# Performance work log

Hardware: AMD Instinct MI355X
Metric: run time of the kernel (lower is better)

The kernel has to match this reference:

```python
import jax, jax.numpy as jnp
import numpy as np

D_MODEL = 1024
NHEAD = 16
D_K = D_MODEL // NHEAD


def setup_inputs() -> dict:
    key = jax.random.key(0)
    ks = jax.random.split(key, 12)
    B, S = 1, 4096
    s = 1.0 / np.sqrt(D_MODEL)
    inp = {
        "query": jax.random.normal(ks[0], (B, S, D_MODEL), jnp.float32),
        "key": jax.random.normal(ks[1], (B, S, D_MODEL), jnp.float32),
        "value": jax.random.normal(ks[2], (B, S, D_MODEL), jnp.float32),
        "W_q": jax.random.normal(ks[3], (D_MODEL, D_MODEL), jnp.float32) * s,
        "b_q": jnp.zeros((D_MODEL,), jnp.float32),
        "W_k": jax.random.normal(ks[4], (D_MODEL, D_MODEL), jnp.float32) * s,
        "b_k": jnp.zeros((D_MODEL,), jnp.float32),
        "W_v": jax.random.normal(ks[5], (D_MODEL, D_MODEL), jnp.float32) * s,
        "b_v": jnp.zeros((D_MODEL,), jnp.float32),
        "W_o": jax.random.normal(ks[6], (D_MODEL, D_MODEL), jnp.float32) * s,
        "b_o": jnp.zeros((D_MODEL,), jnp.float32),
    }
    return inp


def reference(query, key, value, W_q, b_q, W_k, b_k, W_v, b_v, W_o, b_o):
    B, S, _ = query.shape
    # linear projections (torch Linear: x @ W.T + b)
    Q = query @ W_q.T + b_q
    K = key @ W_k.T + b_k
    V = value @ W_v.T + b_v
    # split heads: [B, S, D] -> [B, H, S, d_k]
    Q = Q.reshape(B, S, NHEAD, D_K).transpose(0, 2, 1, 3)
    K = K.reshape(B, S, NHEAD, D_K).transpose(0, 2, 1, 3)
    V = V.reshape(B, S, NHEAD, D_K).transpose(0, 2, 1, 3)
    # scaled dot-product attention (materializes [B,H,S,S] like original)
    scores = jnp.einsum("bhqd,bhkd->bhqk", Q, K) / jnp.sqrt(jnp.float32(D_K))
    weights = jax.nn.softmax(scores, axis=-1)
    attn = jnp.einsum("bhqk,bhkd->bhqd", weights, V)
    # combine heads: [B, H, S, d_k] -> [B, S, D]
    attn = attn.transpose(0, 2, 1, 3).reshape(B, S, D_MODEL)
    return attn @ W_o.T + b_o
```

## Files before the change

kernel.cpp:

```cpp
#include <hip/hip_runtime.h>
#include <hip/hip_bf16.h>
#include <type_traits>

constexpr int SEQ = 4096;
constexpr int DMODEL = 1024;
constexpr int NH = 16;
constexpr int DKH = 64;
constexpr float SCALE = 0.125f;
constexpr float SCALE2 = 0.125f * 1.4426950408889634f;

typedef __bf16 bf16x8 __attribute__((ext_vector_type(8)));
typedef __bf16 bf16x4 __attribute__((ext_vector_type(4)));
typedef float f32x4 __attribute__((ext_vector_type(4)));
typedef float f32x16 __attribute__((ext_vector_type(16)));
typedef unsigned int u32x4 __attribute__((ext_vector_type(4)));
union W8 { u32x4 u; bf16x8 v; };

__device__ inline void store_c(__hip_bfloat16* p, float v) { *p = __float2bfloat16(v); }
__device__ inline void store_c(float* p, float v) { *p = v; }

typedef const void __attribute__((address_space(1)))* gas_ptr;
typedef void __attribute__((address_space(3)))* las_ptr;
__device__ inline void load_lds_16B(const void* g, void* l) {
  __builtin_amdgcn_global_load_lds((gas_ptr)g, (las_ptr)l, 16, 0, 0);
}

__device__ inline unsigned pack2(float a, float b) {
  union { __bf16 h[2]; unsigned u; } p;
  p.h[0] = (__bf16)a; p.h[1] = (__bf16)b;
  return p.u;
}

__device__ inline void st8(__hip_bfloat16* buf, int row, int col, bf16x8 v) {
  *(bf16x8*)(buf + row * 64 + (col ^ ((row & 7) << 3))) = v;
}
__device__ inline bf16x8 ld8(const __hip_bfloat16* buf, int row, int col) {
  return *(const bf16x8*)(buf + row * 64 + (col ^ ((row & 7) << 3)));
}

__global__ __launch_bounds__(256)
void cvt_all(const float* __restrict__ q, const float* __restrict__ k,
             const float* __restrict__ v, const float* __restrict__ wq,
             const float* __restrict__ wk, const float* __restrict__ wv,
             const float* __restrict__ wo,
             __bf16* __restrict__ Xq, __bf16* __restrict__ Xk,
             __bf16* __restrict__ Xv, __bf16* __restrict__ Wqb,
             __bf16* __restrict__ Wkb, __bf16* __restrict__ Wvb,
             __bf16* __restrict__ Wob) {
  const int b = blockIdx.x;
  const float* src; __bf16* dst; size_t base;
  if      (b < 2048) { src = q;  dst = Xq;  base = b; }
  else if (b < 4096) { src = k;  dst = Xk;  base = b - 2048; }
  else if (b < 6144) { src = v;  dst = Xv;  base = b - 4096; }
  else if (b < 6656) { src = wq; dst = Wqb; base = b - 6144; }
  else if (b < 7168) { src = wk; dst = Wkb; base = b - 6656; }
  else if (b < 7680) { src = wv; dst = Wvb; base = b - 7168; }
  else               { src = wo; dst = Wob; base = b - 7680; }
  const size_t i = (base * 256 + threadIdx.x) * 8;
  const float4 a = *(const float4*)(src + i);
  const float4 c = *(const float4*)(src + i + 4);
  bf16x8 r = {(__bf16)a.x, (__bf16)a.y, (__bf16)a.z, (__bf16)a.w,
              (__bf16)c.x, (__bf16)c.y, (__bf16)c.z, (__bf16)c.w};
  *(bf16x8*)(dst + i) = r;
}

constexpr int BK = 64;

template <typename TC, bool TRANS_C>
__global__ __launch_bounds__(256)
void gemm128(const __bf16* __restrict__ A,
             const __bf16* __restrict__ W,
             const float* __restrict__ bias,
             TC* __restrict__ C,
             float out_scale) {
  __shared__ alignas(16) __bf16 As[128][64];
  __shared__ alignas(16) __bf16 Ws[64][64];

  const int t = threadIdx.x;
  const int lane = t & 63;
  const int w = t >> 6;
  const int wr = w >> 1;
  const int wc = w & 1;
  const int col = lane & 15;
  const int quad = lane >> 4;
  const int m_blk = blockIdx.y * 128;
  const int n_blk = blockIdx.x * 64;

  const int srow = t >> 3;
  const int scol = (t & 7) * 8;

  f32x4 acc[4][2] = {};

  for (int k0 = 0; k0 < DMODEL; k0 += BK) {
    __syncthreads();
    #pragma unroll
    for (int p = 0; p < 4; ++p)
      load_lds_16B(A + (size_t)(m_blk + p * 32 + srow) * DMODEL + k0 + scol,
                   &As[p * 32 + srow][scol]);
    #pragma unroll
    for (int p = 0; p < 2; ++p)
      load_lds_16B(W + (size_t)(n_blk + p * 32 + srow) * DMODEL + k0 + scol,
                   &Ws[p * 32 + srow][scol]);
    __syncthreads();

    #pragma unroll
    for (int kh = 0; kh < BK; kh += 32) {
      bf16x8 af[4], bfr[2];
      #pragma unroll
      for (int at = 0; at < 4; ++at)
        af[at] = *(const bf16x8*)&As[wr * 64 + at * 16 + col][kh + quad * 8];
      #pragma unroll
      for (int bt = 0; bt < 2; ++bt)
        bfr[bt] = *(const bf16x8*)&Ws[wc * 32 + bt * 16 + col][kh + quad * 8];
      #pragma unroll
      for (int at = 0; at < 4; ++at)
        #pragma unroll
        for (int bt = 0; bt < 2; ++bt)
          acc[at][bt] = __builtin_amdgcn_mfma_f32_16x16x32_bf16(
              af[at], bfr[bt], acc[at][bt], 0, 0, 0);
    }
  }

  #pragma unroll
  for (int at = 0; at < 4; ++at) {
    #pragma unroll
    for (int bt = 0; bt < 2; ++bt) {
      const int n = n_blk + wc * 32 + bt * 16 + col;
      const float b = bias[n];
      #pragma unroll
      for (int i = 0; i < 4; ++i) {
        const int m = m_blk + wr * 64 + at * 16 + quad * 4 + i;
        const float v = (acc[at][bt][i] + b) * out_scale;
        if constexpr (TRANS_C) store_c(&C[(size_t)n * SEQ + m], v);
        else                   store_c(&C[(size_t)m * DMODEL + n], v);
      }
    }
  }
}

__global__ __launch_bounds__(256)
void gemm_qkv(const __bf16* __restrict__ Xq, const __bf16* __restrict__ Xk,
              const __bf16* __restrict__ Xv, const __bf16* __restrict__ Wq,
              const __bf16* __restrict__ Wk, const __bf16* __restrict__ Wv,
              const float* __restrict__ bq, const float* __restrict__ bk,
              const float* __restrict__ bv,
              __hip_bfloat16* __restrict__ Cq, __hip_bfloat16* __restrict__ Ck,
              __hip_bfloat16* __restrict__ Cv) {
  __shared__ alignas(16) __bf16 As[128][64];
  __shared__ alignas(16) __bf16 Ws[64][64];

  const int z = blockIdx.z;
  const __bf16* A = (z == 0) ? Xq : (z == 1) ? Xk : Xv;
  const __bf16* W = (z == 0) ? Wq : (z == 1) ? Wk : Wv;
  const float* bias = (z == 0) ? bq : (z == 1) ? bk : bv;
  __hip_bfloat16* C = (z == 0) ? Cq : (z == 1) ? Ck : Cv;
  const float out_scale = (z == 0) ? SCALE2 : 1.0f;

  const int t = threadIdx.x;
  const int lane = t & 63;
  const int w = t >> 6;
  const int wr = w >> 1;
  const int wc = w & 1;
  const int col = lane & 15;
  const int quad = lane >> 4;
  const int m_blk = blockIdx.y * 128;
  const int n_blk = blockIdx.x * 64;

  const int srow = t >> 3;
  const int scol = (t & 7) * 8;

  f32x4 acc[4][2] = {};

  for (int k0 = 0; k0 < DMODEL; k0 += BK) {
    __syncthreads();
    #pragma unroll
    for (int p = 0; p < 4; ++p)
      load_lds_16B(A + (size_t)(m_blk + p * 32 + srow) * DMODEL + k0 + scol,
                   &As[p * 32 + srow][scol]);
    #pragma unroll
    for (int p = 0; p < 2; ++p)
      load_lds_16B(W + (size_t)(n_blk + p * 32 + srow) * DMODEL + k0 + scol,
                   &Ws[p * 32 + srow][scol]);
    __syncthreads();

    #pragma unroll
    for (int kh = 0; kh < BK; kh += 32) {
      bf16x8 af[4], bfr[2];
      #pragma unroll
      for (int at = 0; at < 4; ++at)
        af[at] = *(const bf16x8*)&As[wr * 64 + at * 16 + col][kh + quad * 8];
      #pragma unroll
      for (int bt = 0; bt < 2; ++bt)
        bfr[bt] = *(const bf16x8*)&Ws[wc * 32 + bt * 16 + col][kh + quad * 8];
      #pragma unroll
      for (int at = 0; at < 4; ++at)
        #pragma unroll
        for (int bt = 0; bt < 2; ++bt)
          acc[at][bt] = __builtin_amdgcn_mfma_f32_16x16x32_bf16(
              af[at], bfr[bt], acc[at][bt], 0, 0, 0);
    }
  }

  #pragma unroll
  for (int at = 0; at < 4; ++at) {
    #pragma unroll
    for (int bt = 0; bt < 2; ++bt) {
      const int n = n_blk + wc * 32 + bt * 16 + col;
      const float b = bias[n];
      #pragma unroll
      for (int i = 0; i < 4; ++i) {
        const int m = m_blk + wr * 64 + at * 16 + quad * 4 + i;
        const float v = (acc[at][bt][i] + b) * out_scale;
        if (z == 2) *(&C[(size_t)n * SEQ + m]) = __float2bfloat16(v);
        else        *(&C[(size_t)m * DMODEL + n]) = __float2bfloat16(v);
      }
    }
  }
}

constexpr int LDK = 72;

template <typename TA, typename TC, bool TRANS_C>
__global__ __launch_bounds__(256)
void gemm_tiled(const TA* __restrict__ A,
                const float* __restrict__ W,
                const float* __restrict__ bias,
                TC* __restrict__ C,
                float out_scale) {
  __shared__ alignas(16) __bf16 As[128][LDK];
  __shared__ alignas(16) __bf16 Ws[64][LDK];

  const int t = threadIdx.x;
  const int lane = t & 63;
  const int w = t >> 6;
  const int wr = w >> 1;
  const int wc = w & 1;
  const int col = lane & 15;
  const int quad = lane >> 4;
  const int m_blk = blockIdx.y * 128;
  const int n_blk = blockIdx.x * 64;

  f32x4 acc[4][2] = {};

  for (int k0 = 0; k0 < DMODEL; k0 += BK) {
    __syncthreads();
    if constexpr (std::is_same<TA, float>::value) {
      #pragma unroll
      for (int p = 0; p < 8; ++p) {
        const int r = p * 16 + (t >> 4);
        const int c = (t & 15) * 4;
        const float4 v =
            *(const float4*)(A + (size_t)(m_blk + r) * DMODEL + k0 + c);
        bf16x4 b = {(__bf16)v.x, (__bf16)v.y, (__bf16)v.z, (__bf16)v.w};
        *(bf16x4*)&As[r][c] = b;
      }
    } else {
      #pragma unroll
      for (int p = 0; p < 4; ++p) {
        const int r = p * 32 + (t >> 3);
        const int c = (t & 7) * 8;
        *(bf16x8*)&As[r][c] =
            *(const bf16x8*)((const __bf16*)A + (size_t)(m_blk + r) * DMODEL + k0 + c);
      }
    }
    #pragma unroll
    for (int p = 0; p < 4; ++p) {
      const int r = p * 16 + (t >> 4);
      const int c = (t & 15) * 4;
      const float4 v =
          *(const float4*)(W + (size_t)(n_blk + r) * DMODEL + k0 + c);
      bf16x4 b = {(__bf16)v.x, (__bf16)v.y, (__bf16)v.z, (__bf16)v.w};
      *(bf16x4*)&Ws[r][c] = b;
    }
    __syncthreads();

    #pragma unroll
    for (int kh = 0; kh < BK; kh += 32) {
      bf16x8 af[4], bfr[2];
      #pragma unroll
      for (int at = 0; at < 4; ++at)
        af[at] = *(const bf16x8*)&As[wr * 64 + at * 16 + col][kh + quad * 8];
      #pragma unroll
      for (int bt = 0; bt < 2; ++bt)
        bfr[bt] = *(const bf16x8*)&Ws[wc * 32 + bt * 16 + col][kh + quad * 8];
      #pragma unroll
      for (int at = 0; at < 4; ++at)
        #pragma unroll
        for (int bt = 0; bt < 2; ++bt)
          acc[at][bt] = __builtin_amdgcn_mfma_f32_16x16x32_bf16(
              af[at], bfr[bt], acc[at][bt], 0, 0, 0);
    }
  }

  #pragma unroll
  for (int at = 0; at < 4; ++at) {
    #pragma unroll
    for (int bt = 0; bt < 2; ++bt) {
      const int n = n_blk + wc * 32 + bt * 16 + col;
      const float b = bias[n];
      #pragma unroll
      for (int i = 0; i < 4; ++i) {
        const int m = m_blk + wr * 64 + at * 16 + quad * 4 + i;
        const float v = (acc[at][bt][i] + b) * out_scale;
        if constexpr (TRANS_C) store_c(&C[(size_t)n * SEQ + m], v);
        else                   store_c(&C[(size_t)m * DMODEL + n], v);
      }
    }
  }
}

__global__ __launch_bounds__(256, 4)
void flash_attn_split32(const __hip_bfloat16* __restrict__ Q,
                        const __hip_bfloat16* __restrict__ K,
                        const __hip_bfloat16* __restrict__ Vt,
                        __hip_bfloat16* __restrict__ Opart,
                        float* __restrict__ lsum_g) {
  __shared__ alignas(16) __hip_bfloat16 kt[64 * 64];
  __shared__ alignas(16) __hip_bfloat16 vtt[64 * 64];

  const int t = threadIdx.x;
  const int lane = t & 63;
  const int w = t >> 6;
  const int head = blockIdx.y;
  const int q0 = blockIdx.x * 128;
  const int z = blockIdx.z;
  const int l31 = lane & 31;
  const int hl = lane >> 5;

  bf16x8 qf[4];
  {
    const __hip_bfloat16* qp =
        Q + (size_t)(q0 + w * 32 + l31) * DMODEL + head * DKH + hl * 8;
    #pragma unroll
    for (int db = 0; db < 4; ++db) qf[db] = *(const bf16x8*)(qp + db * 16);
  }

  f32x16 acc_o[2] = {};
  float lsa = 0.f, lsb = 0.f;

  const int sr = t >> 2;
  const int sc = (t & 3) * 16;
  const int kbeg = z * (SEQ / 2);
  constexpr int NT = (SEQ / 2) / 64;

  const __hip_bfloat16* kgp = K + (size_t)(kbeg + sr) * DMODEL + head * DKH + sc;
  const __hip_bfloat16* vgp = Vt + (size_t)(head * DKH + sr) * SEQ + kbeg + sc;

  bf16x8 kr0 = *(const bf16x8*)kgp;
  bf16x8 kr1 = *(const bf16x8*)(kgp + 8);
  bf16x8 vr0 = *(const bf16x8*)vgp;
  bf16x8 vr1 = *(const bf16x8*)(vgp + 8);

  for (int ti = 0; ti < NT; ++ti) {
    __syncthreads();
    st8(kt, sr, sc, kr0);  st8(kt, sr, sc + 8, kr1);
    st8(vtt, sr, sc, vr0); st8(vtt, sr, sc + 8, vr1);
    __syncthreads();

    if (ti + 1 < NT) {
      const __hip_bfloat16* kn = kgp + (size_t)(ti + 1) * 64 * DMODEL;
      const __hip_bfloat16* vn = vgp + (ti + 1) * 64;
      kr0 = *(const bf16x8*)kn; kr1 = *(const bf16x8*)(kn + 8);
      vr0 = *(const bf16x8*)vn; vr1 = *(const bf16x8*)(vn + 8);
    }

    bf16x8 pa[4];
    #pragma unroll
    for (int kb = 0; kb < 2; ++kb) {
      f32x16 s = {};
      __builtin_amdgcn_s_setprio(1);
      #pragma unroll
      for (int db = 0; db < 4; ++db) {
        const bf16x8 kf = ld8(kt, kb * 32 + l31, db * 16 + hl * 8);
        s = __builtin_amdgcn_mfma_f32_32x32x16_bf16(kf, qf[db], s, 0, 0, 0);
      }
      __builtin_amdgcn_s_setprio(0);
      unsigned wp[8];
      #pragma unroll
      for (int i = 0; i < 8; ++i) {
        const float p0 = __builtin_amdgcn_exp2f(s[2 * i]);
        const float p1 = __builtin_amdgcn_exp2f(s[2 * i + 1]);
        lsa += p0; lsb += p1;
        wp[i] = pack2(p0, p1);
      }
      #pragma unroll
      for (int b = 0; b < 2; ++b) {
        unsigned a0 = wp[4 * b + 0], a2 = wp[4 * b + 2];
        unsigned a1 = wp[4 * b + 1], a3 = wp[4 * b + 3];
        asm("v_permlane32_swap_b32 %0, %1" : "+v"(a0), "+v"(a2));
        asm("v_permlane32_swap_b32 %0, %1" : "+v"(a1), "+v"(a3));
        W8 u;
        u.u[0] = a0; u.u[1] = a1; u.u[2] = a2; u.u[3] = a3;
        pa[kb * 2 + b] = u.v;
      }
    }

    __builtin_amdgcn_s_setprio(1);
    #pragma unroll
    for (int db = 0; db < 2; ++db)
      #pragma unroll
      for (int kq = 0; kq < 4; ++kq) {
        const bf16x8 vb = ld8(vtt, db * 32 + l31, kq * 16 + hl * 8);
        acc_o[db] = __builtin_amdgcn_mfma_f32_32x32x16_bf16(
            pa[kq], vb, acc_o[db], 0, 0, 0);
      }
    __builtin_amdgcn_s_setprio(0);
  }

  float lsumq = lsa + lsb;
  lsumq += __shfl_xor(lsumq, 32);
  if (lane < 32)
    lsum_g[((size_t)z * NH + head) * SEQ + q0 + w * 32 + lane] = lsumq;

  __hip_bfloat16* O = Opart + (size_t)z * SEQ * DMODEL;
  #pragma unroll
  for (int db = 0; db < 2; ++db) {
    #pragma unroll
    for (int r = 0; r < 16; ++r) {
      const int qr = q0 + w * 32 + (r & 3) + 8 * (r >> 2) + 4 * hl;
      const int c = head * DKH + db * 32 + l31;
      O[(size_t)qr * DMODEL + c] = __float2bfloat16(acc_o[db][r]);
    }
  }
}

__global__ __launch_bounds__(256)
void attn_combine(const __hip_bfloat16* __restrict__ Op,
                  const float* __restrict__ ls,
                  __hip_bfloat16* __restrict__ Ao) {
  const size_t i = ((size_t)blockIdx.x * 256 + threadIdx.x) * 8;
  const int qrow = (int)(i >> 10);
  const int h = (int)((i & 1023) >> 6);
  const float inv = 1.f / (ls[(size_t)h * SEQ + qrow] +
                           ls[(size_t)(NH + h) * SEQ + qrow]);
  const bf16x8 a = *(const bf16x8*)(Op + i);
  const bf16x8 b = *(const bf16x8*)(Op + (size_t)SEQ * DMODEL + i);
  bf16x8 r;
  #pragma unroll
  for (int j = 0; j < 8; ++j)
    r[j] = (__bf16)(((float)a[j] + (float)b[j]) * inv);
  *(bf16x8*)(Ao + i) = r;
}

constexpr int LDP = 72;
constexpr float SHIFT = 8.0f;

__global__ __launch_bounds__(256)
void flash_attn_mono(const __hip_bfloat16* __restrict__ Q,
                     const __hip_bfloat16* __restrict__ K,
                     const __hip_bfloat16* __restrict__ Vt,
                     __hip_bfloat16* __restrict__ O) {
  __shared__ alignas(16) __hip_bfloat16 kt[64][LDP];
  __shared__ alignas(16) __hip_bfloat16 vtt[DKH][LDP];
  __shared__ alignas(16) __hip_bfloat16 plT[4][32][LDP];

  const int t = threadIdx.x;
  const int lane = t & 63;
  const int w = t >> 6;
  const int h = blockIdx.y;
  const int q0 = blockIdx.x * 128;
  const int col = lane & 15;
  const int quad = lane >> 4;

  bf16x8 qf[2][2];
  #pragma unroll
  for (int rg = 0; rg < 2; ++rg) {
    const __hip_bfloat16* qptr =
        Q + (size_t)(q0 + w * 32 + rg * 16 + col) * DMODEL + h * DKH + quad * 8;
    qf[rg][0] = *(const bf16x8*)qptr;
    qf[rg][1] = *(const bf16x8*)(qptr + 32);
  }

  f32x4 acc_o[2][4] = {};
  float lsumq[2] = {0.f, 0.f};
  const int sr = t >> 2;
  const int sc = (t & 3) * 16;

  for (int k0 = 0; k0 < SEQ; k0 += 64) {
    __syncthreads();
    const __hip_bfloat16* kg = K + (size_t)(k0 + sr) * DMODEL + h * DKH + sc;
    *(bf16x8*)&kt[sr][sc]     = *(const bf16x8*)kg;
    *(bf16x8*)&kt[sr][sc + 8] = *(const bf16x8*)(kg + 8);
    const __hip_bfloat16* vg = Vt + (size_t)(h * DKH + sr) * SEQ + k0 + sc;
    *(bf16x8*)&vtt[sr][sc]     = *(const bf16x8*)vg;
    *(bf16x8*)&vtt[sr][sc + 8] = *(const bf16x8*)(vg + 8);
    __syncthreads();

    #pragma unroll
    for (int jt = 0; jt < 4; ++jt) {
      const bf16x8 kf0 = *(const bf16x8*)&kt[jt * 16 + col][quad * 8];
      const bf16x8 kf1 = *(const bf16x8*)&kt[jt * 16 + col][quad * 8 + 32];
      #pragma unroll
      for (int rg = 0; rg < 2; ++rg) {
        f32x4 zz = {0.f, 0.f, 0.f, 0.f};
        zz = __builtin_amdgcn_mfma_f32_16x16x32_bf16(kf0, qf[rg][0], zz, 0, 0, 0);
        zz = __builtin_amdgcn_mfma_f32_16x16x32_bf16(kf1, qf[rg][1], zz, 0, 0, 0);
        bf16x4 pk;
        #pragma unroll
        for (int r = 0; r < 4; ++r) {
          const float p = __expf(zz[r] - SHIFT);
          lsumq[rg] += p;
          pk[r] = (__bf16)p;
        }
        *(bf16x4*)&plT[w][rg * 16 + col][jt * 16 + quad * 4] = pk;
      }
    }

    bf16x8 pa[2][2];
    #pragma unroll
    for (int rg = 0; rg < 2; ++rg) {
      pa[rg][0] = *(const bf16x8*)&plT[w][rg * 16 + col][quad * 8];
      pa[rg][1] = *(const bf16x8*)&plT[w][rg * 16 + col][quad * 8 + 32];
    }
    #pragma unroll
    for (int jt = 0; jt < 4; ++jt) {
      const bf16x8 vb0 = *(const bf16x8*)&vtt[jt * 16 + col][quad * 8];
      const bf16x8 vb1 = *(const bf16x8*)&vtt[jt * 16 + col][quad * 8 + 32];
      #pragma unroll
      for (int rg = 0; rg < 2; ++rg) {
        acc_o[rg][jt] = __builtin_amdgcn_mfma_f32_16x16x32_bf16(
            pa[rg][0], vb0, acc_o[rg][jt], 0, 0, 0);
        acc_o[rg][jt] = __builtin_amdgcn_mfma_f32_16x16x32_bf16(
            pa[rg][1], vb1, acc_o[rg][jt], 0, 0, 0);
      }
    }
  }

  #pragma unroll
  for (int rg = 0; rg < 2; ++rg) {
    lsumq[rg] += __shfl_xor(lsumq[rg], 16);
    lsumq[rg] += __shfl_xor(lsumq[rg], 32);
  }
  float invr[2][4];
  #pragma unroll
  for (int rg = 0; rg < 2; ++rg)
    #pragma unroll
    for (int r = 0; r < 4; ++r)
      invr[rg][r] = 1.f / __shfl(lsumq[rg], quad * 4 + r);

  #pragma unroll
  for (int rg = 0; rg < 2; ++rg) {
    #pragma unroll
    for (int jt = 0; jt < 4; ++jt) {
      #pragma unroll
      for (int r = 0; r < 4; ++r) {
        const int qr = q0 + w * 32 + rg * 16 + quad * 4 + r;
        const int c = h * DKH + jt * 16 + col;
        O[(size_t)qr * DMODEL + c] = __float2bfloat16(acc_o[rg][jt][r] * invr[rg][r]);
      }
    }
  }
}

extern "C" void kernel_launch(void* const* d_in, const int* in_sizes, int n_in,
                              void* d_out, int out_size, void* d_ws, size_t ws_size,
                              hipStream_t stream) {
  const float* query = (const float*)d_in[0];
  const float* key   = (const float*)d_in[1];
  const float* value = (const float*)d_in[2];
  const float* W_q   = (const float*)d_in[3];
  const float* b_q   = (const float*)d_in[4];
  const float* W_k   = (const float*)d_in[5];
  const float* b_k   = (const float*)d_in[6];
  const float* W_v   = (const float*)d_in[7];
  const float* b_v   = (const float*)d_in[8];
  const float* W_o   = (const float*)d_in[9];
  const float* b_o   = (const float*)d_in[10];

  float* out = (float*)d_out;
  const size_t mat = (size_t)SEQ * DMODEL;
  const size_t MB = 1024 * 1024;

  char* ws = (char*)d_ws;
  __hip_bfloat16* Qp = (__hip_bfloat16*)d_out;
  __hip_bfloat16* Kp = (__hip_bfloat16*)ws;
  __hip_bfloat16* Vt = Kp + mat;

  dim3 gblock(256);

  if (ws_size >= 40 * MB) {
    __bf16* Xq  = (__bf16*)((char*)d_out + 8 * MB);
    __bf16* Xk  = (__bf16*)(ws + 16 * MB);
    __bf16* Xv  = (__bf16*)(ws + 24 * MB);
    __bf16* Wqb = (__bf16*)(ws + 32 * MB);
    __bf16* Wkb = (__bf16*)(ws + 34 * MB);
    __bf16* Wvb = (__bf16*)(ws + 36 * MB);
    __bf16* Wob = (__bf16*)(ws + 38 * MB);
    __hip_bfloat16* Opart = (__hip_bfloat16*)(ws + 16 * MB);
    float* lsum = (float*)(ws + 32 * MB);
    __hip_bfloat16* Ao = (__hip_bfloat16*)(ws + 16 * MB);

    hipLaunchKernelGGL(cvt_all, dim3(8192), gblock, 0, stream,
                       query, key, value, W_q, W_k, W_v, W_o,
                       Xq, Xk, Xv, Wqb, Wkb, Wvb, Wob);

    dim3 qkvgrid(DMODEL / 64, SEQ / 128, 3);
    hipLaunchKernelGGL(gemm_qkv, qkvgrid, gblock, 0, stream,
                       Xq, Xk, Xv, Wqb, Wkb, Wvb, b_q, b_k, b_v,
                       Qp, Kp, Vt);

    dim3 agrid(SEQ / 128, NH, 2);
    hipLaunchKernelGGL(flash_attn_split32, agrid, gblock, 0, stream,
                       Qp, Kp, Vt, Opart, lsum);
    hipLaunchKernelGGL(attn_combine, dim3(2048), gblock, 0, stream,
                       Opart, lsum, Ao);

    dim3 ogrid(DMODEL / 64, SEQ / 128);
    hipLaunchKernelGGL((gemm128<float, false>), ogrid, gblock, 0, stream,
                       (const __bf16*)Ao, Wob, b_o, out, 1.0f);
  } else {
    __hip_bfloat16* Ao = Qp + mat;
    float* Cw = (float*)d_ws;
    dim3 fgrid(DMODEL / 64, SEQ / 128);
    hipLaunchKernelGGL((gemm_tiled<float, __hip_bfloat16, false>), fgrid, gblock,
                       0, stream, query, W_q, b_q, Qp, SCALE);
    hipLaunchKernelGGL((gemm_tiled<float, __hip_bfloat16, false>), fgrid, gblock,
                       0, stream, key, W_k, b_k, Kp, 1.0f);
    hipLaunchKernelGGL((gemm_tiled<float, __hip_bfloat16, true>), fgrid, gblock,
                       0, stream, value, W_v, b_v, Vt, 1.0f);
    dim3 agrid(SEQ / 128, NH);
    hipLaunchKernelGGL(flash_attn_mono, agrid, gblock, 0, stream, Qp, Kp, Vt, Ao);
    hipLaunchKernelGGL((gemm_tiled<__hip_bfloat16, float, false>), fgrid, gblock,
                       0, stream, Ao, W_o, b_o, Cw, 1.0f);
    hipMemcpyAsync(out, Cw, mat * sizeof(float), hipMemcpyDeviceToDevice, stream);
  }
}
```

Before: 276.4 us.

## Generalize split-K flash attention to four key segments when workspace allows

Lets the flash attention kernel split the key sequence into a runtime number of segments (four when the workspace holds at least 48MB, otherwise two), each writing a separate partial output buffer that the combine kernel sums. This raises the attention grid from 1024 to 2048 blocks to fill the GPU better, at the cost of more partial-output traffic and a heavier combine step. It also swaps the loop order of the PV MFMA loop. Whether the four-way path runs depends on the workspace size the harness supplies.

Result: no change. 278.1 us (+0.6%).

```diff
diff --git a/kernel.cpp b/kernel.cpp
--- a/kernel.cpp
+++ b/kernel.cpp
@@ -211,8 +211,8 @@
       for (int i = 0; i < 4; ++i) {
         const int m = m_blk + wr * 64 + at * 16 + quad * 4 + i;
         const float v = (acc[at][bt][i] + b) * out_scale;
-        if (z == 2) *(&C[(size_t)n * SEQ + m]) = __float2bfloat16(v);
-        else        *(&C[(size_t)m * DMODEL + n]) = __float2bfloat16(v);
+        if (z == 2) C[(size_t)n * SEQ + m] = __float2bfloat16(v);
+        else        C[(size_t)m * DMODEL + n] = __float2bfloat16(v);
       }
     }
   }
@@ -310,11 +310,14 @@
 }
 
 __global__ __launch_bounds__(256, 4)
-void flash_attn_split32(const __hip_bfloat16* __restrict__ Q,
-                        const __hip_bfloat16* __restrict__ K,
-                        const __hip_bfloat16* __restrict__ Vt,
-                        __hip_bfloat16* __restrict__ Opart,
-                        float* __restrict__ lsum_g) {
+void flash_attn_splitN(const __hip_bfloat16* __restrict__ Q,
+                       const __hip_bfloat16* __restrict__ K,
+                       const __hip_bfloat16* __restrict__ Vt,
+                       __hip_bfloat16* __restrict__ Op0,
+                       __hip_bfloat16* __restrict__ Op1,
+                       __hip_bfloat16* __restrict__ Op2,
+                       __hip_bfloat16* __restrict__ Op3,
+                       float* __restrict__ lsum_g) {
   __shared__ alignas(16) __hip_bfloat16 kt[64 * 64];
   __shared__ alignas(16) __hip_bfloat16 vtt[64 * 64];
 
@@ -324,8 +327,11 @@
   const int head = blockIdx.y;
   const int q0 = blockIdx.x * 128;
   const int z = blockIdx.z;
+  const int nz = gridDim.z;
   const int l31 = lane & 31;
   const int hl = lane >> 5;
+
+  __hip_bfloat16* O = (z == 0) ? Op0 : (z == 1) ? Op1 : (z == 2) ? Op2 : Op3;
 
   bf16x8 qf[4];
   {
@@ -340,8 +346,9 @@
 
   const int sr = t >> 2;
   const int sc = (t & 3) * 16;
-  const int kbeg = z * (SEQ / 2);
-  constexpr int NT = (SEQ / 2) / 64;
+  const int seg = SEQ / nz;
+  const int NT = seg / 64;
+  const int kbeg = z * seg;
 
   const __hip_bfloat16* kgp = K + (size_t)(kbeg + sr) * DMODEL + head * DKH + sc;
   const __hip_bfloat16* vgp = Vt + (size_t)(head * DKH + sr) * SEQ + kbeg + sc;
@@ -397,9 +404,9 @@
 
     __builtin_amdgcn_s_setprio(1);
     #pragma unroll
-    for (int db = 0; db < 2; ++db)
-      #pragma unroll
-      for (int kq = 0; kq < 4; ++kq) {
+    for (int kq = 0; kq < 4; ++kq)
+      #pragma unroll
+      for (int db = 0; db < 2; ++db) {
         const bf16x8 vb = ld8(vtt, db * 32 + l31, kq * 16 + hl * 8);
         acc_o[db] = __builtin_amdgcn_mfma_f32_32x32x16_bf16(
             pa[kq], vb, acc_o[db], 0, 0, 0);
@@ -412,7 +419,6 @@
   if (lane < 32)
     lsum_g[((size_t)z * NH + head) * SEQ + q0 + w * 32 + lane] = lsumq;
 
-  __hip_bfloat16* O = Opart + (size_t)z * SEQ * DMODEL;
   #pragma unroll
   for (int db = 0; db < 2; ++db) {
     #pragma unroll
@@ -425,20 +431,34 @@
 }
 
 __global__ __launch_bounds__(256)
-void attn_combine(const __hip_bfloat16* __restrict__ Op,
+void attn_combine(const __hip_bfloat16* __restrict__ Op0,
+                  const __hip_bfloat16* __restrict__ Op1,
+                  const __hip_bfloat16* __restrict__ Op2,
+                  const __hip_bfloat16* __restrict__ Op3,
                   const float* __restrict__ ls,
-                  __hip_bfloat16* __restrict__ Ao) {
+                  __hip_bfloat16* __restrict__ Ao, int nz) {
   const size_t i = ((size_t)blockIdx.x * 256 + threadIdx.x) * 8;
   const int qrow = (int)(i >> 10);
   const int h = (int)((i & 1023) >> 6);
-  const float inv = 1.f / (ls[(size_t)h * SEQ + qrow] +
-                           ls[(size_t)(NH + h) * SEQ + qrow]);
-  const bf16x8 a = *(const bf16x8*)(Op + i);
-  const bf16x8 b = *(const bf16x8*)(Op + (size_t)SEQ * DMODEL + i);
+  float lsum = ls[(size_t)h * SEQ + qrow] +
+               ls[(size_t)(NH + h) * SEQ + qrow];
+  const bf16x8 a = *(const bf16x8*)(Op0 + i);
+  const bf16x8 b = *(const bf16x8*)(Op1 + i);
+  float s[8];
+  #pragma unroll
+  for (int j = 0; j < 8; ++j) s[j] = (float)a[j] + (float)b[j];
+  if (nz == 4) {
+    lsum += ls[(size_t)(2 * NH + h) * SEQ + qrow] +
+            ls[(size_t)(3 * NH + h) * SEQ + qrow];
+    const bf16x8 c = *(const bf16x8*)(Op2 + i);
+    const bf16x8 d = *(const bf16x8*)(Op3 + i);
+    #pragma unroll
+    for (int j = 0; j < 8; ++j) s[j] += (float)c[j] + (float)d[j];
+  }
+  const float inv = 1.f / lsum;
   bf16x8 r;
   #pragma unroll
-  for (int j = 0; j < 8; ++j)
-    r[j] = (__bf16)(((float)a[j] + (float)b[j]) * inv);
+  for (int j = 0; j < 8; ++j) r[j] = (__bf16)(s[j] * inv);
   *(bf16x8*)(Ao + i) = r;
 }
 
@@ -586,9 +606,14 @@
     __bf16* Wkb = (__bf16*)(ws + 34 * MB);
     __bf16* Wvb = (__bf16*)(ws + 36 * MB);
     __bf16* Wob = (__bf16*)(ws + 38 * MB);
-    __hip_bfloat16* Opart = (__hip_bfloat16*)(ws + 16 * MB);
-    float* lsum = (float*)(ws + 32 * MB);
+    __hip_bfloat16* Op0 = (__hip_bfloat16*)(ws + 16 * MB);
+    __hip_bfloat16* Op1 = (__hip_bfloat16*)(ws + 24 * MB);
+    __hip_bfloat16* Op2 = (__hip_bfloat16*)((char*)d_out + 8 * MB);
+    __hip_bfloat16* Op3 = (__hip_bfloat16*)(ws + 40 * MB);
+    float* lsum = (float*)(ws + 33 * MB);
     __hip_bfloat16* Ao = (__hip_bfloat16*)(ws + 16 * MB);
+
+    const int nz = (ws_size >= 48 * MB) ? 4 : 2;
 
     hipLaunchKernelGGL(cvt_all, dim3(8192), gblock, 0, stream,
                        query, key, value, W_q, W_k, W_v, W_o,
@@ -599,11 +624,11 @@
                        Xq, Xk, Xv, Wqb, Wkb, Wvb, b_q, b_k, b_v,
                        Qp, Kp, Vt);
 
-    dim3 agrid(SEQ / 128, NH, 2);
-    hipLaunchKernelGGL(flash_attn_split32, agrid, gblock, 0, stream,
-                       Qp, Kp, Vt, Opart, lsum);
+    dim3 agrid(SEQ / 128, NH, nz);
+    hipLaunchKernelGGL(flash_attn_splitN, agrid, gblock, 0, stream,
+                       Qp, Kp, Vt, Op0, Op1, Op2, Op3, lsum);
     hipLaunchKernelGGL(attn_combine, dim3(2048), gblock, 0, stream,
-                       Opart, lsum, Ao);
+                       Op0, Op1, Op2, Op3, lsum, Ao, nz);
 
     dim3 ogrid(DMODEL / 64, SEQ / 128);
     hipLaunchKernelGGL((gemm128<float, false>), ogrid, gblock, 0, stream,
```
